# Performance work log

Hardware: AMD Instinct MI355X
Metric: run time of the kernel (lower is better)

Reference implementation:

```python
import jax, jax.numpy as jnp
import numpy as np

N, E, D, H, L = 50000, 800000, 256, 256, 4
EMB = 2 * H  # OGB format: MLP hidden width
BN_EPS = 1e-5


def _bn(h, gamma, beta):
    # training-mode BatchNorm1d: biased batch stats over node dim
    m = jnp.mean(h, axis=0)
    v = jnp.mean((h - m) ** 2, axis=0)
    return gamma * (h - m) / jnp.sqrt(v + BN_EPS) + beta


def setup_inputs() -> dict:
    key = jax.random.key(0)
    ks = jax.random.split(key, 12)
    x = jax.random.normal(ks[0], (N, D), dtype=jnp.float32)
    edge_index = jax.random.randint(ks[1], (2, E), 0, N, dtype=jnp.int64)
    s1 = 1.0 / np.sqrt(D)
    s2 = 1.0 / np.sqrt(EMB)
    return {
        "x": x,
        "edge_index": edge_index,
        "W1": jax.random.uniform(ks[2], (L, D, EMB), jnp.float32, -s1, s1),
        "b1": jax.random.uniform(ks[3], (L, EMB), jnp.float32, -s1, s1),
        "bn1_gamma": jnp.ones((L, EMB), jnp.float32),
        "bn1_beta": jnp.zeros((L, EMB), jnp.float32),
        "W2": jax.random.uniform(ks[4], (L, EMB, H), jnp.float32, -s2, s2),
        "b2": jax.random.uniform(ks[5], (L, H), jnp.float32, -s2, s2),
        "bn2_gamma": jnp.ones((L, H), jnp.float32),
        "bn2_beta": jnp.zeros((L, H), jnp.float32),
    }


def reference(x, edge_index, W1, b1, bn1_gamma, bn1_beta, W2, b2, bn2_gamma, bn2_beta):
    src, dst = edge_index[0], edge_index[1]
    n = x.shape[0]
    h = x
    for l in range(L):
        # GINConv with eps=0: (1+eps)*h_i + sum_{j->i} h_j
        agg = h + jax.ops.segment_sum(h[src], dst, num_segments=n)
        # inner MLP: Linear -> BN -> ReLU -> Linear
        z = jax.nn.relu(_bn(agg @ W1[l] + b1[l], bn1_gamma[l], bn1_beta[l]))
        z = z @ W2[l] + b2[l]
        # outer BN; ReLU except last layer (dropout = identity in eval/reference)
        z = _bn(z, bn2_gamma[l], bn2_beta[l])
        h = z if l == L - 1 else jax.nn.relu(z)
    return h
```

## Files before the change

kernel.cpp:

```cpp
#include <hip/hip_runtime.h>
#include <stdint.h>

#define NN 50000
#define NE 800000
#define DD 256
#define EM 512
#define NL 4
#define EPS 1e-5f

typedef unsigned short u16;
typedef __attribute__((ext_vector_type(4))) unsigned short u16x4;
typedef __attribute__((ext_vector_type(8))) short s16x8;
typedef __attribute__((ext_vector_type(8))) float f32x8;
typedef __attribute__((ext_vector_type(4))) float f32x4;
typedef __attribute__((ext_vector_type(8))) __bf16 bf16x8;

union Frag { s16x8 s; bf16x8 b; };

__device__ __forceinline__ float bf2f(u16 h) {
  unsigned u = ((unsigned)h) << 16;
  return __builtin_bit_cast(float, u);
}
__device__ __forceinline__ u16 f2bf(float f) {
  unsigned u = __builtin_bit_cast(unsigned, f);
  u = (u + 0x7FFFu + ((u >> 16) & 1u)) >> 16;
  return (u16)u;
}
__device__ __forceinline__ void bfsplit(float f, u16& hi, u16& lo) {
  hi = f2bf(f);
  lo = f2bf(f - bf2f(hi));
}

__device__ __forceinline__ void gload16(const u16* g, u16* l) {
  __builtin_amdgcn_global_load_lds(
      (const __attribute__((address_space(1))) unsigned int*)g,
      (__attribute__((address_space(3))) unsigned int*)l, 16, 0, 0);
}


__global__ void k_f32_to_bf16(const float* __restrict__ in, u16* __restrict__ out, int n8) {
  int i = blockIdx.x * blockDim.x + threadIdx.x;
  int stride = gridDim.x * blockDim.x;
  for (; i < n8; i += stride) {
    f32x8 v = ((const f32x8*)in)[i];
    s16x8 o;
#pragma unroll
    for (int j = 0; j < 8; j++) o[j] = (short)f2bf(v[j]);
    ((s16x8*)out)[i] = o;
  }
}

__global__ void k_prep_w(const float* __restrict__ W, u16* __restrict__ WThi,
                         u16* __restrict__ WTlo, int K, int Nc) {
  int total = NL * K * Nc;
  for (int i = blockIdx.x * blockDim.x + threadIdx.x; i < total; i += gridDim.x * blockDim.x) {
    int l = i / (K * Nc);
    int rem = i - l * (K * Nc);
    int k = rem / Nc;
    int n = rem - k * Nc;
    float v = W[i];
    u16 hi, lo; bfsplit(v, hi, lo);
    size_t o = (size_t)l * Nc * K + (size_t)n * K + k;
    WThi[o] = hi; WTlo[o] = lo;
  }
}

__global__ void k_deg(const int* __restrict__ dst, int* __restrict__ deg) {
  for (int e = blockIdx.x * blockDim.x + threadIdx.x; e < NE; e += gridDim.x * blockDim.x)
    atomicAdd(&deg[dst[e]], 1);
}

__global__ __launch_bounds__(1024) void k_scan(const int* __restrict__ deg, int* __restrict__ rowptr) {
  __shared__ int part[1024];
  int t = threadIdx.x;
  const int CH = (NN + 1023) / 1024;
  int base = t * CH;
  int s = 0;
  for (int i = 0; i < CH; i++) { int idx = base + i; if (idx < NN) s += deg[idx]; }
  part[t] = s;
  __syncthreads();
  for (int off = 1; off < 1024; off <<= 1) {
    int v = (t >= off) ? part[t - off] : 0;
    __syncthreads();
    part[t] += v;
    __syncthreads();
  }
  int run = part[t] - s;
  for (int i = 0; i < CH; i++) {
    int idx = base + i;
    if (idx < NN) { rowptr[idx] = run; run += deg[idx]; }
  }
  if (t == 1023) rowptr[NN] = part[1023];
}

__global__ void k_fill(const int* __restrict__ src, const int* __restrict__ dst,
                       const int* __restrict__ rowptr, int* __restrict__ cursor,
                       int* __restrict__ cols) {
  for (int e = blockIdx.x * blockDim.x + threadIdx.x; e < NE; e += gridDim.x * blockDim.x) {
    int d = dst[e];
    int pos = atomicAdd(&cursor[d], 1);
    cols[rowptr[d] + pos] = src[e];
  }
}


template <bool FUSED>
__global__ __launch_bounds__(256) void k_agg(const u16* __restrict__ src,
                                             const float* __restrict__ ss,
                                             const int* __restrict__ rowptr,
                                             const int* __restrict__ cols,
                                             u16* __restrict__ Ahi,
                                             u16* __restrict__ Alo) {
  int wid = threadIdx.x >> 6, lane = threadIdx.x & 63;
  int node = blockIdx.x * 4 + wid;
  int c0 = lane << 2;
  f32x4 sc, sh;
  if (FUSED) {
    sc = *(const f32x4*)(ss + c0);
    sh = *(const f32x4*)(ss + DD + c0);
  }
  u16x4 v = *(const u16x4*)(src + (size_t)node * DD + c0);
  f32x4 a;
#pragma unroll
  for (int j = 0; j < 4; j++) {
    float f = bf2f(v[j]);
    a[j] = FUSED ? fmaxf(f * sc[j] + sh[j], 0.f) : f;
  }
  int beg = rowptr[node], end = rowptr[node + 1];
  int e = beg;
  for (; e + 3 < end; e += 4) {
    int s0 = cols[e], s1 = cols[e + 1], s2 = cols[e + 2], s3 = cols[e + 3];
    u16x4 w0 = *(const u16x4*)(src + (size_t)s0 * DD + c0);
    u16x4 w1 = *(const u16x4*)(src + (size_t)s1 * DD + c0);
    u16x4 w2 = *(const u16x4*)(src + (size_t)s2 * DD + c0);
    u16x4 w3 = *(const u16x4*)(src + (size_t)s3 * DD + c0);
#pragma unroll
    for (int j = 0; j < 4; j++) {
      float f0 = bf2f(w0[j]), f1 = bf2f(w1[j]), f2 = bf2f(w2[j]), f3 = bf2f(w3[j]);
      if (FUSED) {
        f0 = fmaxf(f0 * sc[j] + sh[j], 0.f);
        f1 = fmaxf(f1 * sc[j] + sh[j], 0.f);
        f2 = fmaxf(f2 * sc[j] + sh[j], 0.f);
        f3 = fmaxf(f3 * sc[j] + sh[j], 0.f);
      }
      a[j] += f0; a[j] += f1; a[j] += f2; a[j] += f3;
    }
  }
  for (; e < end; ++e) {
    int s = cols[e];
    u16x4 w = *(const u16x4*)(src + (size_t)s * DD + c0);
#pragma unroll
    for (int j = 0; j < 4; j++) {
      float f = bf2f(w[j]);
      a[j] += FUSED ? fmaxf(f * sc[j] + sh[j], 0.f) : f;
    }
  }
  u16x4 oh, ol;
#pragma unroll
  for (int j = 0; j < 4; j++) { u16 hi, lo; bfsplit(a[j], hi, lo); oh[j] = hi; ol[j] = lo; }
  *(u16x4*)(Ahi + (size_t)node * DD + c0) = oh;
  *(u16x4*)(Alo + (size_t)node * DD + c0) = ol;
}

template <int K, int NC, bool OUT_BF16, int NSEG>
__global__ __launch_bounds__(256) void k_gemm(const u16* __restrict__ Ahi,
                                              const u16* __restrict__ Alo,
                                              const u16* __restrict__ WThi,
                                              const u16* __restrict__ WTlo,
                                              const float* __restrict__ bias,
                                              void* __restrict__ Zout,
                                              float* __restrict__ stats, int M) {
  __shared__ u16 AlHi[128 * 32];
  __shared__ u16 AlLo[NSEG == 3 ? 128 * 32 : 64];
  __shared__ u16 BlHi[128 * 32];
  __shared__ u16 BlLo[128 * 32];
  __shared__ float sblk[256];
  int tid = threadIdx.x;
  sblk[tid] = 0.f;
  int lane = tid & 63, wid = tid >> 6;
  int wm = wid & 1, wn = wid >> 1;
  int brow = blockIdx.x * 128;
  int bcol = blockIdx.y * 128;

  f32x4 zero = {0.f, 0.f, 0.f, 0.f};
  f32x4 acc[4][4];
#pragma unroll
  for (int m = 0; m < 4; m++)
#pragma unroll
    for (int n = 0; n < 4; n++) acc[m][n] = zero;

  int rinc = lane >> 2;
  int cq = (lane & 3) * 8;
  long ra0 = brow + wid * 16 + rinc;  if (ra0 > M - 1) ra0 = M - 1;
  long ra1 = brow + 64 + wid * 16 + rinc; if (ra1 > M - 1) ra1 = M - 1;
  long rb0 = bcol + wid * 16 + rinc;
  long rb1 = bcol + 64 + wid * 16 + rinc;

  const u16* gAh0 = Ahi + ra0 * K + cq;
  const u16* gAh1 = Ahi + ra1 * K + cq;
  const u16* gAl0 = Alo + ra0 * K + cq;
  const u16* gAl1 = Alo + ra1 * K + cq;
  const u16* gBh0 = WThi + rb0 * K + cq;
  const u16* gBh1 = WThi + rb1 * K + cq;
  const u16* gBl0 = WTlo + rb0 * K + cq;
  const u16* gBl1 = WTlo + rb1 * K + cq;
  int lc0 = wid * 512, lc1 = (wid + 4) * 512;

  int fr = lane & 15;
  int kk = (lane >> 4) * 8;
  int fo = (wm * 64 + fr) * 32 + kk;
  int go = (wn * 64 + fr) * 32 + kk;

  const int KS = K / 32;
  for (int kt = 0; kt < KS; ++kt) {
    int k0 = kt * 32;
    gload16(gAh0 + k0, &AlHi[lc0]);
    gload16(gAh1 + k0, &AlHi[lc1]);
    if (NSEG == 3) {
      gload16(gAl0 + k0, &AlLo[lc0]);
      gload16(gAl1 + k0, &AlLo[lc1]);
    }
    gload16(gBh0 + k0, &BlHi[lc0]);
    gload16(gBh1 + k0, &BlHi[lc1]);
    gload16(gBl0 + k0, &BlLo[lc0]);
    gload16(gBl1 + k0, &BlLo[lc1]);
    __syncthreads();

    Frag aH[4], bH[4], bL[4];
#pragma unroll
    for (int m = 0; m < 4; m++) aH[m].s = *(const s16x8*)(&AlHi[fo + m * 512]);
#pragma unroll
    for (int n = 0; n < 4; n++) bH[n].s = *(const s16x8*)(&BlHi[go + n * 512]);
#pragma unroll
    for (int n = 0; n < 4; n++) bL[n].s = *(const s16x8*)(&BlLo[go + n * 512]);
#pragma unroll
    for (int m = 0; m < 4; m++)
#pragma unroll
      for (int n = 0; n < 4; n++)
        acc[m][n] = __builtin_amdgcn_mfma_f32_16x16x32_bf16(aH[m].b, bH[n].b, acc[m][n], 0, 0, 0);
    if (NSEG == 3) {
      Frag aL[4];
#pragma unroll
      for (int m = 0; m < 4; m++) aL[m].s = *(const s16x8*)(&AlLo[fo + m * 512]);
#pragma unroll
      for (int m = 0; m < 4; m++)
#pragma unroll
        for (int n = 0; n < 4; n++)
          acc[m][n] = __builtin_amdgcn_mfma_f32_16x16x32_bf16(aL[m].b, bH[n].b, acc[m][n], 0, 0, 0);
    }
#pragma unroll
    for (int m = 0; m < 4; m++)
#pragma unroll
      for (int n = 0; n < 4; n++)
        acc[m][n] = __builtin_amdgcn_mfma_f32_16x16x32_bf16(aH[m].b, bL[n].b, acc[m][n], 0, 0, 0);
    __syncthreads();
  }

  int colb = bcol + wn * 64;
  float bv[4];
#pragma unroll
  for (int n = 0; n < 4; n++) bv[n] = bias[colb + n * 16 + fr];
  int rb = brow + wm * 64 + ((lane >> 4) << 2);
  float sn[4] = {0.f, 0.f, 0.f, 0.f}, qn[4] = {0.f, 0.f, 0.f, 0.f};
#pragma unroll
  for (int m = 0; m < 4; m++) {
#pragma unroll
    for (int r = 0; r < 4; r++) {
      int row = rb + m * 16 + r;
      if (row < M) {
        size_t base = (size_t)row * NC + colb + fr;
#pragma unroll
        for (int n = 0; n < 4; n++) {
          float z = acc[m][n][r] + bv[n];
          if (OUT_BF16) ((u16*)Zout)[base + n * 16] = f2bf(z);
          else          ((float*)Zout)[base + n * 16] = z;
          sn[n] += z; qn[n] += z * z;
        }
      }
    }
  }
#pragma unroll
  for (int n = 0; n < 4; n++) {
    sn[n] += __shfl_xor(sn[n], 16); sn[n] += __shfl_xor(sn[n], 32);
    qn[n] += __shfl_xor(qn[n], 16); qn[n] += __shfl_xor(qn[n], 32);
  }
  if (lane < 16) {
#pragma unroll
    for (int n = 0; n < 4; n++) {
      atomicAdd(&sblk[wn * 64 + n * 16 + lane], sn[n]);
      atomicAdd(&sblk[128 + wn * 64 + n * 16 + lane], qn[n]);
    }
  }
  __syncthreads();
  if (tid < 128) atomicAdd(&stats[bcol + tid], sblk[tid]);
  else           atomicAdd(&stats[NC + bcol + (tid - 128)], sblk[tid]);
}

__global__ void k_finalize(const float* __restrict__ stats, const float* __restrict__ gamma,
                           const float* __restrict__ beta, float* __restrict__ ss, int NC) {
  int c = blockIdx.x * blockDim.x + threadIdx.x;
  if (c < NC) {
    float mean = stats[c] * (1.0f / NN);
    float var = stats[NC + c] * (1.0f / NN) - mean * mean;
    float sc = gamma[c] * rsqrtf(var + EPS);
    ss[c] = sc;
    ss[NC + c] = beta[c] - mean * sc;
  }
}

template <int NC>
__global__ void k_bn_a2(const u16* __restrict__ Z, const float* __restrict__ ss,
                        u16* __restrict__ A2, int n8) {
  int i = blockIdx.x * blockDim.x + threadIdx.x;
  int stride = gridDim.x * blockDim.x;
  for (; i < n8; i += stride) {
    int c = (i * 8) & (NC - 1);
    s16x8 v = *(const s16x8*)(Z + (size_t)i * 8);
    s16x8 o;
#pragma unroll
    for (int j = 0; j < 8; j++) {
      float f = fmaxf(bf2f((u16)v[j]) * ss[c + j] + ss[NC + c + j], 0.f);
      o[j] = (short)f2bf(f);
    }
    *(s16x8*)(A2 + (size_t)i * 8) = o;
  }
}

template <int NC>
__global__ void k_bn_out(const float* __restrict__ Z, const float* __restrict__ ss,
                         float* __restrict__ out, int n4) {
  int i = blockIdx.x * blockDim.x + threadIdx.x;
  int stride = gridDim.x * blockDim.x;
  for (; i < n4; i += stride) {
    int c = (i * 4) & (NC - 1);
    f32x4 v = *(const f32x4*)(Z + (size_t)i * 4);
    f32x4 o;
#pragma unroll
    for (int j = 0; j < 4; j++) o[j] = v[j] * ss[c + j] + ss[NC + c + j];
    *(f32x4*)(out + (size_t)i * 4) = o;
  }
}


extern "C" void kernel_launch(void* const* d_in, const int* in_sizes, int n_in,
                              void* d_out, int out_size, void* d_ws, size_t ws_size,
                              hipStream_t stream) {
  const float* x  = (const float*)d_in[0];
  const int* ei   = (const int*)d_in[1];
  const int* esrc = ei;
  const int* edst = ei + NE;
  const float* W1 = (const float*)d_in[2];
  const float* b1 = (const float*)d_in[3];
  const float* g1 = (const float*)d_in[4];
  const float* be1= (const float*)d_in[5];
  const float* W2 = (const float*)d_in[6];
  const float* b2 = (const float*)d_in[7];
  const float* g2 = (const float*)d_in[8];
  const float* be2= (const float*)d_in[9];
  float* out = (float*)d_out;

  char* w = (char*)d_ws;
  auto alloc = [&](size_t bytes) {
    char* p = w;
    w += (bytes + 255) & ~(size_t)255;
    return p;
  };
  char* R0 = alloc((size_t)NN * EM * 2);
  char* R1 = alloc((size_t)NN * EM * 2);
  u16* W1hi = (u16*)alloc((size_t)NL * EM * DD * 2);
  u16* W1lo = (u16*)alloc((size_t)NL * EM * DD * 2);
  u16* W2hi = (u16*)alloc((size_t)NL * DD * EM * 2);
  u16* W2lo = (u16*)alloc((size_t)NL * DD * EM * 2);
  int* deg    = (int*)alloc((size_t)NN * 4);
  int* rowptr = (int*)alloc((size_t)(NN + 1) * 4);
  int* cursor = (int*)alloc((size_t)NN * 4);
  int* cols   = (int*)alloc((size_t)NE * 4);
  float* stats1 = (float*)alloc(2 * EM * 4);
  float* stats2 = (float*)alloc(2 * DD * 4);
  float* ss1    = (float*)alloc(2 * EM * 4);
  float* ss2    = (float*)alloc(2 * DD * 4);

  u16*   Hb   = (u16*)R0;
  u16*   Z1   = (u16*)R0;
  float* Z2f  = (float*)R0;
  u16*   A1hi = (u16*)R1;
  u16*   A1lo = (u16*)R1 + (size_t)NN * DD;
  u16*   A2   = (u16*)R1;

  hipMemsetAsync(deg, 0, (size_t)NN * 4, stream);
  hipMemsetAsync(cursor, 0, (size_t)NN * 4, stream);
  k_deg<<<2048, 256, 0, stream>>>(edst, deg);
  k_scan<<<1, 1024, 0, stream>>>(deg, rowptr);
  k_fill<<<2048, 256, 0, stream>>>(esrc, edst, rowptr, cursor, cols);
  k_prep_w<<<2048, 256, 0, stream>>>(W1, W1hi, W1lo, DD, EM);
  k_prep_w<<<2048, 256, 0, stream>>>(W2, W2hi, W2lo, EM, DD);
  k_f32_to_bf16<<<2048, 256, 0, stream>>>(x, Hb, NN * DD / 8);

  for (int l = 0; l < NL; ++l) {
    if (l == 0)
      k_agg<false><<<NN / 4, 256, 0, stream>>>(Hb, nullptr, rowptr, cols, A1hi, A1lo);
    else
      k_agg<true><<<NN / 4, 256, 0, stream>>>(Hb, ss2, rowptr, cols, A1hi, A1lo);

    hipMemsetAsync(stats1, 0, 2 * EM * 4, stream);
    k_gemm<DD, EM, true, 3><<<dim3((NN + 127) / 128, EM / 128), 256, 0, stream>>>(
        A1hi, A1lo, W1hi + (size_t)l * EM * DD, W1lo + (size_t)l * EM * DD,
        b1 + (size_t)l * EM, Z1, stats1, NN);
    k_finalize<<<2, 256, 0, stream>>>(stats1, g1 + (size_t)l * EM, be1 + (size_t)l * EM, ss1, EM);
    k_bn_a2<EM><<<2048, 256, 0, stream>>>(Z1, ss1, A2, NN * EM / 8);

    hipMemsetAsync(stats2, 0, 2 * DD * 4, stream);
    if (l < NL - 1) {
      k_gemm<EM, DD, true, 2><<<dim3((NN + 127) / 128, DD / 128), 256, 0, stream>>>(
          A2, A2, W2hi + (size_t)l * DD * EM, W2lo + (size_t)l * DD * EM,
          b2 + (size_t)l * DD, Hb, stats2, NN);
    } else {
      k_gemm<EM, DD, false, 2><<<dim3((NN + 127) / 128, DD / 128), 256, 0, stream>>>(
          A2, A2, W2hi + (size_t)l * DD * EM, W2lo + (size_t)l * DD * EM,
          b2 + (size_t)l * DD, Z2f, stats2, NN);
    }
    k_finalize<<<1, 256, 0, stream>>>(stats2, g2 + (size_t)l * DD, be2 + (size_t)l * DD, ss2, DD);
  }
  k_bn_out<DD><<<2048, 256, 0, stream>>>(Z2f, ss2, out, NN * DD / 4);
}
```

Measured before the change: 1.164 ms.

## Parallelize CSR scan, remap GEMM blocks for L2 locality, consolidate memsets

The single-block serial prefix scan over node degrees becomes a three-kernel multi-block scan. GEMM launches move to a 1D grid that groups eight row-blocks with all their column-blocks, so consecutive blocks share A tiles in cache. Per-layer BN stat buffers are preallocated and zeroed once together with deg and cursor in a single memset, which removes repeated memset calls. The scan adds two extra launches, and the swizzle adds a few early-exit blocks.

```diff
diff --git a/kernel.cpp b/kernel.cpp
--- a/kernel.cpp
+++ b/kernel.cpp
@@ -70,27 +70,44 @@
     atomicAdd(&deg[dst[e]], 1);
 }
 
-__global__ __launch_bounds__(1024) void k_scan(const int* __restrict__ deg, int* __restrict__ rowptr) {
-  __shared__ int part[1024];
-  int t = threadIdx.x;
-  const int CH = (NN + 1023) / 1024;
-  int base = t * CH;
-  int s = 0;
-  for (int i = 0; i < CH; i++) { int idx = base + i; if (idx < NN) s += deg[idx]; }
-  part[t] = s;
+#define SCB 49
+
+__global__ __launch_bounds__(1024) void k_scan1(const int* __restrict__ deg,
+                                                int* __restrict__ rowptr,
+                                                int* __restrict__ part) {
+  __shared__ int sm[1024];
+  int t = threadIdx.x, b = blockIdx.x;
+  int idx = b * 1024 + t;
+  int v = (idx < NN) ? deg[idx] : 0;
+  sm[t] = v;
   __syncthreads();
   for (int off = 1; off < 1024; off <<= 1) {
-    int v = (t >= off) ? part[t - off] : 0;
+    int u = (t >= off) ? sm[t - off] : 0;
     __syncthreads();
-    part[t] += v;
+    sm[t] += u;
     __syncthreads();
   }
-  int run = part[t] - s;
-  for (int i = 0; i < CH; i++) {
-    int idx = base + i;
-    if (idx < NN) { rowptr[idx] = run; run += deg[idx]; }
-  }
-  if (t == 1023) rowptr[NN] = part[1023];
+  int incl = sm[t];
+  if (idx < NN) rowptr[idx] = incl - v;
+  if (t == 1023) part[b] = incl;
+}
+
+__global__ void k_scan2(int* __restrict__ part, int* __restrict__ rowptr) {
+  int t = threadIdx.x;
+  int v = (t < SCB) ? part[t] : 0;
+  int orig = v;
+  for (int off = 1; off < 64; off <<= 1) {
+    int u = __shfl_up(v, off);
+    if (t >= off) v += u;
+  }
+  if (t < SCB) part[t] = v - orig;
+  if (t == SCB - 1) rowptr[NN] = v;
+}
+
+__global__ __launch_bounds__(1024) void k_scan3(int* __restrict__ rowptr,
+                                                const int* __restrict__ part) {
+  int idx = blockIdx.x * 1024 + threadIdx.x;
+  if (idx < NN) rowptr[idx] += part[blockIdx.x];
 }
 
 __global__ void k_fill(const int* __restrict__ src, const int* __restrict__ dst,
@@ -170,6 +187,17 @@
                                               const float* __restrict__ bias,
                                               void* __restrict__ Zout,
                                               float* __restrict__ stats, int M) {
+  constexpr int NCB = NC / 128;
+  int nxb = (M + 127) >> 7;
+  int bid = blockIdx.x;
+  int slot = bid & 7;
+  int ycb  = (bid >> 3) & (NCB - 1);
+  int grp  = bid / (8 * NCB);
+  int xb   = grp * 8 + slot;
+  if (xb >= nxb) return;
+  int brow = xb * 128;
+  int bcol = ycb * 128;
+
   __shared__ u16 AlHi[128 * 32];
   __shared__ u16 AlLo[NSEG == 3 ? 128 * 32 : 64];
   __shared__ u16 BlHi[128 * 32];
@@ -179,8 +207,6 @@
   sblk[tid] = 0.f;
   int lane = tid & 63, wid = tid >> 6;
   int wm = wid & 1, wn = wid >> 1;
-  int brow = blockIdx.x * 128;
-  int bcol = blockIdx.y * 128;
 
   f32x4 zero = {0.f, 0.f, 0.f, 0.f};
   f32x4 acc[4][4];
@@ -371,14 +397,17 @@
   u16* W1lo = (u16*)alloc((size_t)NL * EM * DD * 2);
   u16* W2hi = (u16*)alloc((size_t)NL * DD * EM * 2);
   u16* W2lo = (u16*)alloc((size_t)NL * DD * EM * 2);
-  int* deg    = (int*)alloc((size_t)NN * 4);
+  char* zbase = (char*)alloc((size_t)NN * 4);
+  int* deg    = (int*)zbase;
+  int* cursor = (int*)alloc((size_t)NN * 4);
+  float* stats1 = (float*)alloc((size_t)NL * 2 * EM * 4);
+  float* stats2 = (float*)alloc((size_t)NL * 2 * DD * 4);
+  size_t zspan = (char*)w - zbase;
   int* rowptr = (int*)alloc((size_t)(NN + 1) * 4);
-  int* cursor = (int*)alloc((size_t)NN * 4);
+  int* part   = (int*)alloc(64 * 4);
   int* cols   = (int*)alloc((size_t)NE * 4);
-  float* stats1 = (float*)alloc(2 * EM * 4);
-  float* stats2 = (float*)alloc(2 * DD * 4);
-  float* ss1    = (float*)alloc(2 * EM * 4);
-  float* ss2    = (float*)alloc(2 * DD * 4);
+  float* ss1  = (float*)alloc(2 * EM * 4);
+  float* ss2  = (float*)alloc(2 * DD * 4);
 
   u16*   Hb   = (u16*)R0;
   u16*   Z1   = (u16*)R0;
@@ -387,39 +416,44 @@
   u16*   A1lo = (u16*)R1 + (size_t)NN * DD;
   u16*   A2   = (u16*)R1;
 
-  hipMemsetAsync(deg, 0, (size_t)NN * 4, stream);
-  hipMemsetAsync(cursor, 0, (size_t)NN * 4, stream);
+  hipMemsetAsync(zbase, 0, zspan, stream);
   k_deg<<<2048, 256, 0, stream>>>(edst, deg);
-  k_scan<<<1, 1024, 0, stream>>>(deg, rowptr);
+  k_scan1<<<SCB, 1024, 0, stream>>>(deg, rowptr, part);
+  k_scan2<<<1, 64, 0, stream>>>(part, rowptr);
+  k_scan3<<<SCB, 1024, 0, stream>>>(rowptr, part);
   k_fill<<<2048, 256, 0, stream>>>(esrc, edst, rowptr, cursor, cols);
   k_prep_w<<<2048, 256, 0, stream>>>(W1, W1hi, W1lo, DD, EM);
   k_prep_w<<<2048, 256, 0, stream>>>(W2, W2hi, W2lo, EM, DD);
   k_f32_to_bf16<<<2048, 256, 0, stream>>>(x, Hb, NN * DD / 8);
 
+  const int NXB = (NN + 127) / 128;
+  const int G1GRID = ((NXB + 7) / 8) * 8 * (EM / 128);
+  const int G2GRID = ((NXB + 7) / 8) * 8 * (DD / 128);
+
   for (int l = 0; l < NL; ++l) {
+    float* st1 = stats1 + (size_t)l * 2 * EM;
+    float* st2 = stats2 + (size_t)l * 2 * DD;
     if (l == 0)
       k_agg<false><<<NN / 4, 256, 0, stream>>>(Hb, nullptr, rowptr, cols, A1hi, A1lo);
     else
       k_agg<true><<<NN / 4, 256, 0, stream>>>(Hb, ss2, rowptr, cols, A1hi, A1lo);
 
-    hipMemsetAsync(stats1, 0, 2 * EM * 4, stream);
-    k_gemm<DD, EM, true, 3><<<dim3((NN + 127) / 128, EM / 128), 256, 0, stream>>>(
+    k_gemm<DD, EM, true, 3><<<G1GRID, 256, 0, stream>>>(
         A1hi, A1lo, W1hi + (size_t)l * EM * DD, W1lo + (size_t)l * EM * DD,
-        b1 + (size_t)l * EM, Z1, stats1, NN);
-    k_finalize<<<2, 256, 0, stream>>>(stats1, g1 + (size_t)l * EM, be1 + (size_t)l * EM, ss1, EM);
+        b1 + (size_t)l * EM, Z1, st1, NN);
+    k_finalize<<<2, 256, 0, stream>>>(st1, g1 + (size_t)l * EM, be1 + (size_t)l * EM, ss1, EM);
     k_bn_a2<EM><<<2048, 256, 0, stream>>>(Z1, ss1, A2, NN * EM / 8);
 
-    hipMemsetAsync(stats2, 0, 2 * DD * 4, stream);
     if (l < NL - 1) {
-      k_gemm<EM, DD, true, 2><<<dim3((NN + 127) / 128, DD / 128), 256, 0, stream>>>(
+      k_gemm<EM, DD, true, 2><<<G2GRID, 256, 0, stream>>>(
           A2, A2, W2hi + (size_t)l * DD * EM, W2lo + (size_t)l * DD * EM,
-          b2 + (size_t)l * DD, Hb, stats2, NN);
+          b2 + (size_t)l * DD, Hb, st2, NN);
     } else {
-      k_gemm<EM, DD, false, 2><<<dim3((NN + 127) / 128, DD / 128), 256, 0, stream>>>(
+      k_gemm<EM, DD, false, 2><<<G2GRID, 256, 0, stream>>>(
           A2, A2, W2hi + (size_t)l * DD * EM, W2lo + (size_t)l * DD * EM,
-          b2 + (size_t)l * DD, Z2f, stats2, NN);
-    }
-    k_finalize<<<1, 256, 0, stream>>>(stats2, g2 + (size_t)l * DD, be2 + (size_t)l * DD, ss2, DD);
+          b2 + (size_t)l * DD, Z2f, st2, NN);
+    }
+    k_finalize<<<1, 256, 0, stream>>>(st2, g2 + (size_t)l * DD, be2 + (size_t)l * DD, ss2, DD);
   }
   k_bn_out<DD><<<2048, 256, 0, stream>>>(Z2f, ss2, out, NN * DD / 4);
 }
```

New measurement: 980.3 us. -15.8%, faster.
